# Optimization experiments

Measured on AMD Instinct MI355X. Metric: run time of the kernel, lower is better.

The kernel has to match this reference:

```python
import jax, jax.numpy as jnp
import numpy as np

N = 8192        # number of cells/nodes
D_IN = 30       # input feature dim
P_DIM = 3       # position dim
HID = 32        # attention hidden dim
D_OUT = 30      # backbone output dim
FF = 128        # MLP hidden width
SIGMA = 0.3     # spatial decay sigma


def setup_inputs() -> dict:
    key = jax.random.key(0)
    ks = jax.random.split(key, 12)
    w = lambda k, shape: (jax.random.normal(k, shape, jnp.float32) * 0.1)
    return {
        "t": jax.random.uniform(ks[0], (1,), jnp.float32),
        "Z": jax.random.normal(ks[1], (N, D_IN + P_DIM + 1), jnp.float32),
        # SpatialAttentionLayer params (Q/K/V projections + output proj)
        "Wq": w(ks[2], (D_IN, HID)), "bq": jnp.zeros((HID,), jnp.float32),
        "Wk": w(ks[3], (D_IN, HID)), "bk": jnp.zeros((HID,), jnp.float32),
        "Wv": w(ks[4], (D_IN, HID)), "bv": jnp.zeros((HID,), jnp.float32),
        "Wo": w(ks[5], (HID, D_OUT)), "bo": jnp.zeros((D_OUT,), jnp.float32),
        # LayerNorm
        "ln_g": jnp.ones((D_OUT,), jnp.float32), "ln_b": jnp.zeros((D_OUT,), jnp.float32),
        # backbone MLP: Linear(30,128) -> SiLU -> Linear(128,30)
        "W1": w(ks[6], (D_OUT, FF)), "b1": jnp.zeros((FF,), jnp.float32),
        "W2": w(ks[7], (FF, D_OUT)), "b2": jnp.zeros((D_OUT,), jnp.float32),
        # expr_head: Linear(30,30)
        "We": w(ks[8], (D_OUT, D_OUT)), "be": jnp.zeros((D_OUT,), jnp.float32),
    }


def reference(t, Z, Wq, bq, Wk, bk, Wv, bv, Wo, bo, ln_g, ln_b, W1, b1, W2, b2, We, be):
    # Z: (N, D_IN + P_DIM + 1); last column is kinetic energy (unused in fwd)
    X = Z[:, :-1]                       # (N, 33)
    P = X[:, -P_DIM:]                   # (N, 3) positions
    F = X[:, :D_IN]                     # (N, 30) features

    # --- SpatialAttentionLayer: sigma distance-decay attention, no softmax ---
    Q = F @ Wq + bq
    K = F @ Wk + bk
    V = F @ Wv + bv
    scores = (Q @ K.T) / jnp.sqrt(jnp.float32(HID))          # (N, N)
    pn = jnp.sum(P * P, axis=1)
    d2 = jnp.maximum(pn[:, None] + pn[None, :] - 2.0 * (P @ P.T), 0.0)
    decay = jnp.exp(-d2 / (2.0 * SIGMA * SIGMA))              # spatial decay kernel
    A = jax.nn.sigmoid(scores) * decay                        # no-softmax attention
    A = A / (jnp.sum(A, axis=1, keepdims=True) + 1e-8)        # row-normalized message passing
    H = (A @ V) @ Wo + bo                                     # (N, D_OUT)

    # --- LayerNorm(output_dim) ---
    mu = jnp.mean(H, axis=-1, keepdims=True)
    var = jnp.mean((H - mu) ** 2, axis=-1, keepdims=True)
    Hn = (H - mu) * jax.lax.rsqrt(var + 1e-5) * ln_g + ln_b

    # --- Linear(30,128) -> SiLU -> Linear(128,30) ---
    H2 = jax.nn.silu(Hn @ W1 + b1) @ W2 + b2

    # --- expr_head ---
    feature_velo = H2 @ We + be                               # (N, 30)

    # static_pos=True -> zero position velocities (velocity_head bypassed)
    pos_velo = jnp.zeros_like(P)                              # (N, 3)

    # kinetic energy term
    ke = 0.5 * jnp.mean(feature_velo ** 2, axis=1) + 0.5 * jnp.mean(pos_velo ** 2, axis=1)
    return jnp.concatenate([feature_velo, pos_velo, ke[:, None]], axis=1)  # (N, 34)
```

## Files before the change

### kernel.cpp

```cpp
#include <hip/hip_runtime.h>
#include <hip/hip_bf16.h>

#define N      8192
#define D_IN   30
#define HID    32
#define D_OUT  30
#define FFD    128
#define ZC     34
#define JGC    16

typedef __attribute__((ext_vector_type(8))) short short8;
typedef __attribute__((ext_vector_type(16))) float f32x16;

static __device__ __forceinline__ ushort f2bf(float x) {
    uint32_t u = __float_as_uint(x);
    uint32_t r = (u + 0x7fffu + ((u >> 16) & 1u)) >> 16;
    return (ushort)r;
}
static __device__ __forceinline__ float bf2f(ushort u) {
    return __uint_as_float(((uint32_t)u) << 16);
}

__global__ __launch_bounds__(256) void dv_qkv_kernel(
    const float* __restrict__ Z,
    const float* __restrict__ Wq, const float* __restrict__ bq,
    const float* __restrict__ Wk, const float* __restrict__ bk,
    const float* __restrict__ Wv, const float* __restrict__ bv,
    const float* __restrict__ Wo,
    const float* __restrict__ W2, const float* __restrict__ We,
    const float* __restrict__ b2, const float* __restrict__ be,
    ushort* __restrict__ Qb, ushort* __restrict__ Kb,
    ushort* __restrict__ VWot, ushort* __restrict__ KA,
    ushort* __restrict__ QB, float* __restrict__ W2e, float* __restrict__ b2e)
{
    __shared__ ushort sv[8][33];
    const int t = blockIdx.x * 256 + threadIdx.x;
    const int i = t >> 5;
    const int h = t & 31;
    const float* z = Z + (size_t)i * ZC;

    float q = bq[h], k = bk[h], v = bv[h];
#pragma unroll
    for (int d = 0; d < D_IN; ++d) {
        float zf = z[d];
        q = fmaf(zf, Wq[d * HID + h], q);
        k = fmaf(zf, Wk[d * HID + h], k);
        v = fmaf(zf, Wv[d * HID + h], v);
    }
    const float QS = 0.17677669529663687f * 1.4426950408889634f;
    Qb[(size_t)i * HID + h] = f2bf(q * QS);
    Kb[(size_t)i * HID + h] = f2bf(k);
    sv[threadIdx.x >> 5][h] = f2bf(v);

    if (h == 0) {
        float p0 = z[D_IN], p1 = z[D_IN + 1], p2 = z[D_IN + 2];
        const float C2 = 1.4426950408889634f / 0.18f;
        const float SC = sqrtf(2.0f * C2);
        float px = p0 * SC, py = p1 * SC, pz = p2 * SC;
        float w  = -C2 * (p0 * p0 + p1 * p1 + p2 * p2);
        ushort phx = f2bf(px), phy = f2bf(py), phz = f2bf(pz);
        ushort plx = f2bf(px - bf2f(phx));
        ushort ply = f2bf(py - bf2f(phy));
        ushort plz = f2bf(pz - bf2f(phz));
        ushort wh  = f2bf(w);
        ushort wl  = f2bf(w - bf2f(wh));
        ushort nhx = phx ^ 0x8000, nhy = phy ^ 0x8000, nhz = phz ^ 0x8000;
        ushort nlx = plx ^ 0x8000, nly = ply ^ 0x8000, nlz = plz ^ 0x8000;
        ushort nwh = wh ^ 0x8000,  nwl = wl ^ 0x8000;
        const ushort one = 0x3F80, none = 0xBF80;
        ushort ka0[8] = {nwh, nwl, none, none, nhx, nhy, nhz, nhx};
        ushort ka1[8] = {nhy, nhz, nlx, nly, nlz, nlx, nly, nlz};
        ushort qb0[8] = {one, one, wh, wl, phx, phy, phz, plx};
        ushort qb1[8] = {ply, plz, phx, phy, phz, plx, ply, plz};
        *(uint4*)&KA[(size_t)i * 8]       = *(uint4*)ka0;
        *(uint4*)&KA[((size_t)N + i) * 8] = *(uint4*)ka1;
        *(uint4*)&QB[(size_t)i * 8]       = *(uint4*)qb0;
        *(uint4*)&QB[((size_t)N + i) * 8] = *(uint4*)qb1;
    }

    if (blockIdx.x < 15) {
        int idx = blockIdx.x * 256 + threadIdx.x;
        int f = idx / 30, o = idx - f * 30;
        float acc = 0.f;
#pragma unroll
        for (int d = 0; d < D_OUT; ++d)
            acc = fmaf(W2[f * D_OUT + d], We[d * D_OUT + o], acc);
        W2e[idx] = acc;
        if (idx < D_OUT) {
            float a2 = be[idx];
#pragma unroll
            for (int d = 0; d < D_OUT; ++d)
                a2 = fmaf(b2[d], We[d * D_OUT + idx], a2);
            b2e[idx] = a2;
        }
    }

    __syncthreads();
    const int io = threadIdx.x >> 5, c = threadIdx.x & 31;
    const int ii = blockIdx.x * 8 + io;
    float val;
    if (c < 30) {
        float acc = 0.f;
#pragma unroll
        for (int hh = 0; hh < HID; ++hh)
            acc = fmaf(bf2f(sv[io][hh]), Wo[hh * D_OUT + c], acc);
        val = acc;
    } else {
        val = (c == 31) ? 1.0f : 0.f;
    }
    VWot[(size_t)c * N + ii] = f2bf(val);
}

__global__ __launch_bounds__(256, 2) void dv_attn_kernel(
    const ushort* __restrict__ Qb, const ushort* __restrict__ Kb,
    const ushort* __restrict__ VWot, const ushort* __restrict__ KA,
    const ushort* __restrict__ QB, float* __restrict__ partial, int nch)
{
    __shared__ ushort lK[128 * 32];
    __shared__ ushort lV[32 * 128];
    __shared__ ushort lKA[2][128 * 8];

    const int tid  = threadIdx.x;
    const int lane = tid & 63;
    const int wv   = tid >> 6;
    const int h2   = lane >> 5;
    const int l31  = lane & 31;
    const int rb   = blockIdx.x & 63;
    const int jg   = blockIdx.x >> 6;
    const int i0w  = rb * 128 + wv * 32;

    const ushort* qp = Qb + (size_t)(i0w + l31) * HID + h2 * 8;
    const short8 qf0 = *(const short8*)qp;
    const short8 qf1 = *(const short8*)(qp + 16);
    const short8 qaug = *(const short8*)&QB[((size_t)h2 * N + i0w + l31) * 8];

    f32x16 zacc, oacc;
#pragma unroll
    for (int r = 0; r < 16; ++r) { zacc[r] = 0.f; oacc[r] = 0.f; }

    const int cA0 = (h2 + (l31 >> 1)) & 3;
    const int cA1 = (cA0 + 2) & 3;

    const int kjr0 = tid >> 2,          kcc0 = tid & 3;
    const int kjr1 = (tid + 256) >> 2,  kcc1 = (tid + 256) & 3;
    const int kc20 = (kcc0 + (kjr0 >> 1)) & 3;
    const int kc21 = (kcc1 + (kjr1 >> 1)) & 3;
    const int vhh[4] = { tid >> 5, (tid + 256) >> 5, (tid + 512) >> 5, (tid + 768) >> 5 };
    const int vcc[4] = { tid & 31, tid & 31, tid & 31, tid & 31 };
    const int ahalf = tid >> 7, ajj = tid & 127;

    uint4 kreg[2];
    uint2 vreg[4];
    uint4 kareg;

    {
        const int j0 = (jg * nch) << 7;
        kreg[0] = *(const uint4*)&Kb[(size_t)(j0 + kjr0) * HID + kcc0 * 8];
        kreg[1] = *(const uint4*)&Kb[(size_t)(j0 + kjr1) * HID + kcc1 * 8];
#pragma unroll
        for (int r2 = 0; r2 < 4; ++r2)
            vreg[r2] = *(const uint2*)&VWot[(size_t)vhh[r2] * N + j0 + vcc[r2] * 4];
        kareg = *(const uint4*)&KA[((size_t)ahalf * N + j0 + ajj) * 8];
    }

    for (int ch = 0; ch < nch; ++ch) {
        __syncthreads();
        *(uint4*)&lK[kjr0 * 32 + kc20 * 8] = kreg[0];
        *(uint4*)&lK[kjr1 * 32 + kc21 * 8] = kreg[1];
#pragma unroll
        for (int r2 = 0; r2 < 4; ++r2)
            *(uint2*)&lV[vhh[r2] * 128 + (vcc[r2] ^ vhh[r2]) * 4] = vreg[r2];
        *(uint4*)&lKA[ahalf][ajj * 8] = kareg;
        __syncthreads();

        if (ch + 1 < nch) {
            const int j1 = (jg * nch + ch + 1) << 7;
            kreg[0] = *(const uint4*)&Kb[(size_t)(j1 + kjr0) * HID + kcc0 * 8];
            kreg[1] = *(const uint4*)&Kb[(size_t)(j1 + kjr1) * HID + kcc1 * 8];
#pragma unroll
            for (int r2 = 0; r2 < 4; ++r2)
                vreg[r2] = *(const uint2*)&VWot[(size_t)vhh[r2] * N + j1 + vcc[r2] * 4];
            kareg = *(const uint4*)&KA[((size_t)ahalf * N + j1 + ajj) * 8];
        }

#pragma unroll
        for (int t32 = 0; t32 < 4; ++t32) {
            const ushort* krow = &lK[(t32 * 32 + l31) * 32];
            short8 kf0 = *(const short8*)&krow[cA0 * 8];
            short8 kf1 = *(const short8*)&krow[cA1 * 8];
            f32x16 s = __builtin_amdgcn_mfma_f32_32x32x16_bf16(kf0, qf0, zacc, 0, 0, 0);
            s = __builtin_amdgcn_mfma_f32_32x32x16_bf16(kf1, qf1, s, 0, 0, 0);

            short8 kaug = *(const short8*)&lKA[h2][(t32 * 32 + l31) * 8];
            f32x16 gA = __builtin_amdgcn_mfma_f32_32x32x16_bf16(kaug, qaug, zacc, 0, 0, 0);

            uint32_t pk[8];
#pragma unroll
            for (int p = 0; p < 8; ++p) {
                float d0 = fmaxf(gA[2 * p], 0.f);
                float d1 = fmaxf(gA[2 * p + 1], 0.f);
                float eg0 = __builtin_amdgcn_exp2f(-d0);
                float es0 = __builtin_amdgcn_exp2f(-s[2 * p]);
                float a0  = eg0 * __builtin_amdgcn_rcpf(1.0f + es0);
                float eg1 = __builtin_amdgcn_exp2f(-d1);
                float es1 = __builtin_amdgcn_exp2f(-s[2 * p + 1]);
                float a1  = eg1 * __builtin_amdgcn_rcpf(1.0f + es1);
                asm("v_cvt_pk_bf16_f32 %0, %1, %2" : "=v"(pk[p]) : "v"(a0), "v"(a1));
            }
            union BV { uint32_t u[4]; short8 v; };
            BV fa, fb;
            fa.u[0] = pk[0]; fa.u[1] = pk[1]; fa.u[2] = pk[2]; fa.u[3] = pk[3];
            fb.u[0] = pk[4]; fb.u[1] = pk[5]; fb.u[2] = pk[6]; fb.u[3] = pk[7];

            const ushort* vrow = &lV[l31 * 128];
            const int cb = t32 * 8 + h2;
            BV b0, b1;
            *(uint2*)&b0.u[0] = *(const uint2*)&vrow[((cb    ) ^ l31) * 4];
            *(uint2*)&b0.u[2] = *(const uint2*)&vrow[((cb + 2) ^ l31) * 4];
            *(uint2*)&b1.u[0] = *(const uint2*)&vrow[((cb + 4) ^ l31) * 4];
            *(uint2*)&b1.u[2] = *(const uint2*)&vrow[((cb + 6) ^ l31) * 4];

            oacc = __builtin_amdgcn_mfma_f32_32x32x16_bf16(fa.v, b0.v, oacc, 0, 0, 0);
            oacc = __builtin_amdgcn_mfma_f32_32x32x16_bf16(fb.v, b1.v, oacc, 0, 0, 0);
        }
    }

#pragma unroll
    for (int r = 0; r < 16; ++r) {
        int ir = (r & 3) + 8 * (r >> 2) + 4 * h2 + i0w;
        partial[(size_t)ir * (JGC * 32) + jg * 32 + l31] = oacc[r];
    }
}

__global__ __launch_bounds__(256) void dv_epilogue_kernel(
    const float* __restrict__ partial,
    const float* __restrict__ bo,
    const float* __restrict__ ln_g, const float* __restrict__ ln_b,
    const float* __restrict__ W1, const float* __restrict__ b1,
    const float* __restrict__ W2e, const float* __restrict__ b2e,
    float* __restrict__ out)
{
    __shared__ float sr [32 * 16];
    __shared__ float sHl[30 * 16];
    __shared__ float sHn[30 * 16];
    __shared__ float shf[128 * 16];
    __shared__ float sker[16 * 16];

    const int tid  = threadIdx.x;
    const int row0 = blockIdx.x * 16;

#pragma unroll
    for (int rep = 0; rep < 2; ++rep) {
        int idx = tid + rep * 256;
        int r = idx >> 5, c = idx & 31;
        const float* pp = partial + (size_t)(row0 + r) * (JGC * 32) + c;
        float s = 0.f;
#pragma unroll
        for (int jg = 0; jg < JGC; ++jg)
            s += pp[jg * 32];
        sr[c * 16 + r] = s;
    }
    __syncthreads();

    const int rl  = tid & 15, grp = tid >> 4;
    const int o0  = grp * 2;
    const bool g15 = grp < 15;

    if (g15) {
        float inv = __builtin_amdgcn_rcpf(sr[31 * 16 + rl] + 1e-8f);
        float2 bb = *(const float2*)&bo[o0];
        sHl[(o0    ) * 16 + rl] = fmaf(sr[(o0    ) * 16 + rl], inv, bb.x);
        sHl[(o0 + 1) * 16 + rl] = fmaf(sr[(o0 + 1) * 16 + rl], inv, bb.y);
    }
    __syncthreads();

    if (tid < 16) {
        const int r = tid;
        float mu = 0.f;
#pragma unroll
        for (int o = 0; o < D_OUT; ++o) mu += sHl[o * 16 + r];
        mu *= (1.0f / D_OUT);
        float var = 0.f;
#pragma unroll
        for (int o = 0; o < D_OUT; ++o) {
            float d = sHl[o * 16 + r] - mu; var = fmaf(d, d, var);
        }
        float rs = rsqrtf(var * (1.0f / D_OUT) + 1e-5f);
#pragma unroll
        for (int o = 0; o < D_OUT; ++o)
            sHn[o * 16 + r] = fmaf((sHl[o * 16 + r] - mu) * rs, ln_g[o], ln_b[o]);
    }
    __syncthreads();

    {
        const int f0 = grp * 8;
        float acc[8];
        float4 b4a = *(const float4*)&b1[f0];
        float4 b4b = *(const float4*)&b1[f0 + 4];
        acc[0] = b4a.x; acc[1] = b4a.y; acc[2] = b4a.z; acc[3] = b4a.w;
        acc[4] = b4b.x; acc[5] = b4b.y; acc[6] = b4b.z; acc[7] = b4b.w;
#pragma unroll
        for (int o = 0; o < D_OUT; ++o) {
            float4 wa = *(const float4*)&W1[o * FFD + f0];
            float4 wb = *(const float4*)&W1[o * FFD + f0 + 4];
            float hn = sHn[o * 16 + rl];
            acc[0] = fmaf(hn, wa.x, acc[0]); acc[1] = fmaf(hn, wa.y, acc[1]);
            acc[2] = fmaf(hn, wa.z, acc[2]); acc[3] = fmaf(hn, wa.w, acc[3]);
            acc[4] = fmaf(hn, wb.x, acc[4]); acc[5] = fmaf(hn, wb.y, acc[5]);
            acc[6] = fmaf(hn, wb.z, acc[6]); acc[7] = fmaf(hn, wb.w, acc[7]);
        }
        const float L2E = 1.4426950408889634f;
#pragma unroll
        for (int ff = 0; ff < 8; ++ff) {
            float a = acc[ff];
            shf[(f0 + ff) * 16 + rl] =
                a * __builtin_amdgcn_rcpf(1.0f + __builtin_amdgcn_exp2f(-a * L2E));
        }
    }
    __syncthreads();

    if (g15) {
        float2 bb = *(const float2*)&b2e[o0];
        float a0 = bb.x, a1 = bb.y;
#pragma unroll 8
        for (int f = 0; f < FFD; ++f) {
            float2 w = *(const float2*)&W2e[f * D_OUT + o0];
            float hf = shf[f * 16 + rl];
            a0 = fmaf(hf, w.x, a0); a1 = fmaf(hf, w.y, a1);
        }
        float* op = out + (size_t)(row0 + rl) * ZC;
        op[o0] = a0; op[o0 + 1] = a1;
        sker[grp * 16 + rl] = fmaf(a0, a0, a1 * a1);
    }
    __syncthreads();

    if (tid < 16) {
        float ke = 0.f;
#pragma unroll
        for (int g = 0; g < 15; ++g) ke += sker[g * 16 + tid];
        float* op = out + (size_t)(row0 + tid) * ZC;
        op[30] = 0.f; op[31] = 0.f; op[32] = 0.f;
        op[33] = ke * (0.5f / D_OUT);
    }
}

extern "C" void kernel_launch(void* const* d_in, const int* in_sizes, int n_in,
                              void* d_out, int out_size, void* d_ws, size_t ws_size,
                              hipStream_t stream)
{
    const float* Z  = (const float*)d_in[1];
    const float* Wq = (const float*)d_in[2];
    const float* bq = (const float*)d_in[3];
    const float* Wk = (const float*)d_in[4];
    const float* bk = (const float*)d_in[5];
    const float* Wv = (const float*)d_in[6];
    const float* bv = (const float*)d_in[7];
    const float* Wo = (const float*)d_in[8];
    const float* bo = (const float*)d_in[9];
    const float* lg = (const float*)d_in[10];
    const float* lb = (const float*)d_in[11];
    const float* W1 = (const float*)d_in[12];
    const float* b1 = (const float*)d_in[13];
    const float* W2 = (const float*)d_in[14];
    const float* b2 = (const float*)d_in[15];
    const float* We = (const float*)d_in[16];
    const float* be = (const float*)d_in[17];
    float* out = (float*)d_out;

    ushort* Qb   = (ushort*)d_ws;
    ushort* Kb   = Qb + (size_t)N * HID;
    ushort* VWot = Kb + (size_t)N * HID;
    ushort* KA   = VWot + (size_t)N * HID;
    ushort* QB   = KA + (size_t)N * 16;
    float*  W2e  = (float*)(QB + (size_t)N * 16);
    float*  b2e  = W2e + FFD * D_OUT;
    float*  partial = b2e + 32;

    int nch = N / (JGC * 128);

    hipLaunchKernelGGL(dv_qkv_kernel, dim3((N * HID) / 256), dim3(256), 0, stream,
                       Z, Wq, bq, Wk, bk, Wv, bv, Wo, W2, We, b2, be,
                       Qb, Kb, VWot, KA, QB, W2e, b2e);
    hipLaunchKernelGGL(dv_attn_kernel, dim3(64 * JGC), dim3(256), 0, stream,
                       Qb, Kb, VWot, KA, QB, partial, nch);
    hipLaunchKernelGGL(dv_epilogue_kernel, dim3(N / 16), dim3(256), 0, stream,
                       partial, bo, lg, lb, W1, b1, W2e, b2e, out);
}
```

Measured before the change: 61.77 us.

## Rewrite epilogue as one wavefront per row and drop the distance clamp

Measured after the change: 58.44 us. -5.4%, faster.

```diff
diff --git a/kernel.cpp b/kernel.cpp
--- a/kernel.cpp
+++ b/kernel.cpp
@@ -19,6 +19,9 @@
 }
 static __device__ __forceinline__ float bf2f(ushort u) {
     return __uint_as_float(((uint32_t)u) << 16);
+}
+static __device__ __forceinline__ float rdlane(float v, int l) {
+    return __uint_as_float(__builtin_amdgcn_readlane(__float_as_uint(v), l));
 }
 
 __global__ __launch_bounds__(256) void dv_qkv_kernel(
@@ -146,7 +149,7 @@
     const int kc20 = (kcc0 + (kjr0 >> 1)) & 3;
     const int kc21 = (kcc1 + (kjr1 >> 1)) & 3;
     const int vhh[4] = { tid >> 5, (tid + 256) >> 5, (tid + 512) >> 5, (tid + 768) >> 5 };
-    const int vcc[4] = { tid & 31, tid & 31, tid & 31, tid & 31 };
+    const int vcx = tid & 31;
     const int ahalf = tid >> 7, ajj = tid & 127;
 
     uint4 kreg[2];
@@ -159,7 +162,7 @@
         kreg[1] = *(const uint4*)&Kb[(size_t)(j0 + kjr1) * HID + kcc1 * 8];
 #pragma unroll
         for (int r2 = 0; r2 < 4; ++r2)
-            vreg[r2] = *(const uint2*)&VWot[(size_t)vhh[r2] * N + j0 + vcc[r2] * 4];
+            vreg[r2] = *(const uint2*)&VWot[(size_t)vhh[r2] * N + j0 + vcx * 4];
         kareg = *(const uint4*)&KA[((size_t)ahalf * N + j0 + ajj) * 8];
     }
 
@@ -169,7 +172,7 @@
         *(uint4*)&lK[kjr1 * 32 + kc21 * 8] = kreg[1];
 #pragma unroll
         for (int r2 = 0; r2 < 4; ++r2)
-            *(uint2*)&lV[vhh[r2] * 128 + (vcc[r2] ^ vhh[r2]) * 4] = vreg[r2];
+            *(uint2*)&lV[vhh[r2] * 128 + (vcx ^ vhh[r2]) * 4] = vreg[r2];
         *(uint4*)&lKA[ahalf][ajj * 8] = kareg;
         __syncthreads();
 
@@ -179,7 +182,7 @@
             kreg[1] = *(const uint4*)&Kb[(size_t)(j1 + kjr1) * HID + kcc1 * 8];
 #pragma unroll
             for (int r2 = 0; r2 < 4; ++r2)
-                vreg[r2] = *(const uint2*)&VWot[(size_t)vhh[r2] * N + j1 + vcc[r2] * 4];
+                vreg[r2] = *(const uint2*)&VWot[(size_t)vhh[r2] * N + j1 + vcx * 4];
             kareg = *(const uint4*)&KA[((size_t)ahalf * N + j1 + ajj) * 8];
         }
 
@@ -197,12 +200,10 @@
             uint32_t pk[8];
 #pragma unroll
             for (int p = 0; p < 8; ++p) {
-                float d0 = fmaxf(gA[2 * p], 0.f);
-                float d1 = fmaxf(gA[2 * p + 1], 0.f);
-                float eg0 = __builtin_amdgcn_exp2f(-d0);
+                float eg0 = __builtin_amdgcn_exp2f(-gA[2 * p]);
                 float es0 = __builtin_amdgcn_exp2f(-s[2 * p]);
                 float a0  = eg0 * __builtin_amdgcn_rcpf(1.0f + es0);
-                float eg1 = __builtin_amdgcn_exp2f(-d1);
+                float eg1 = __builtin_amdgcn_exp2f(-gA[2 * p + 1]);
                 float es1 = __builtin_amdgcn_exp2f(-s[2 * p + 1]);
                 float a1  = eg1 * __builtin_amdgcn_rcpf(1.0f + es1);
                 asm("v_cvt_pk_bf16_f32 %0, %1, %2" : "=v"(pk[p]) : "v"(a0), "v"(a1));
@@ -240,107 +241,78 @@
     const float* __restrict__ W2e, const float* __restrict__ b2e,
     float* __restrict__ out)
 {
-    __shared__ float sr [32 * 16];
-    __shared__ float sHl[30 * 16];
-    __shared__ float sHn[30 * 16];
-    __shared__ float shf[128 * 16];
-    __shared__ float sker[16 * 16];
+    __shared__ float shf[4][FFD];
 
     const int tid  = threadIdx.x;
-    const int row0 = blockIdx.x * 16;
-
-#pragma unroll
-    for (int rep = 0; rep < 2; ++rep) {
-        int idx = tid + rep * 256;
-        int r = idx >> 5, c = idx & 31;
-        const float* pp = partial + (size_t)(row0 + r) * (JGC * 32) + c;
-        float s = 0.f;
-#pragma unroll
-        for (int jg = 0; jg < JGC; ++jg)
-            s += pp[jg * 32];
-        sr[c * 16 + r] = s;
-    }
-    __syncthreads();
-
-    const int rl  = tid & 15, grp = tid >> 4;
-    const int o0  = grp * 2;
-    const bool g15 = grp < 15;
-
-    if (g15) {
-        float inv = __builtin_amdgcn_rcpf(sr[31 * 16 + rl] + 1e-8f);
-        float2 bb = *(const float2*)&bo[o0];
-        sHl[(o0    ) * 16 + rl] = fmaf(sr[(o0    ) * 16 + rl], inv, bb.x);
-        sHl[(o0 + 1) * 16 + rl] = fmaf(sr[(o0 + 1) * 16 + rl], inv, bb.y);
-    }
-    __syncthreads();
-
-    if (tid < 16) {
-        const int r = tid;
-        float mu = 0.f;
-#pragma unroll
-        for (int o = 0; o < D_OUT; ++o) mu += sHl[o * 16 + r];
-        mu *= (1.0f / D_OUT);
-        float var = 0.f;
-#pragma unroll
-        for (int o = 0; o < D_OUT; ++o) {
-            float d = sHl[o * 16 + r] - mu; var = fmaf(d, d, var);
+    const int wv   = tid >> 6;
+    const int lane = tid & 63;
+    const int row  = blockIdx.x * 4 + wv;
+    const int c    = lane & 31;
+    const bool a30 = c < 30;
+    const int  c30 = a30 ? c : 0;
+
+    float s8 = 0.f;
+    {
+        const float* pp = partial + (size_t)row * (JGC * 32) + lane;
+#pragma unroll
+        for (int q = 0; q < 8; ++q) s8 += pp[q * 64];
+    }
+    float sv = s8 + __shfl_xor(s8, 32, 64);
+
+    float rsum = __shfl(sv, 31, 32);
+    float inv  = __builtin_amdgcn_rcpf(rsum + 1e-8f);
+    float Hl   = a30 ? fmaf(sv, inv, bo[c30]) : 0.f;
+
+    float x = Hl;
+#pragma unroll
+    for (int m = 1; m < 32; m <<= 1) x += __shfl_xor(x, m, 32);
+    float mu = x * (1.0f / D_OUT);
+    float d  = a30 ? (Hl - mu) : 0.f;
+    float v2 = d * d;
+#pragma unroll
+    for (int m = 1; m < 32; m <<= 1) v2 += __shfl_xor(v2, m, 32);
+    float rs = rsqrtf(v2 * (1.0f / D_OUT) + 1e-5f);
+    float Hn = fmaf(d * rs, ln_g[c30], ln_b[c30]);
+
+    float acc0 = b1[lane], acc1 = b1[lane + 64];
+#pragma unroll
+    for (int o = 0; o < D_OUT; ++o) {
+        float ho = rdlane(Hn, o);
+        acc0 = fmaf(ho, W1[o * FFD + lane], acc0);
+        acc1 = fmaf(ho, W1[o * FFD + lane + 64], acc1);
+    }
+    const float L2E = 1.4426950408889634f;
+    shf[wv][lane] =
+        acc0 * __builtin_amdgcn_rcpf(1.0f + __builtin_amdgcn_exp2f(-acc0 * L2E));
+    shf[wv][lane + 64] =
+        acc1 * __builtin_amdgcn_rcpf(1.0f + __builtin_amdgcn_exp2f(-acc1 * L2E));
+
+    const int half = lane >> 5;
+    float acc = 0.f;
+    {
+        const float* hbase = &shf[wv][half * 64];
+#pragma unroll
+        for (int k = 0; k < 16; ++k) {
+            float4 hv = *(const float4*)&hbase[k * 4];
+            const int f0 = half * 64 + k * 4;
+            acc = fmaf(hv.x, W2e[(f0    ) * D_OUT + c30], acc);
+            acc = fmaf(hv.y, W2e[(f0 + 1) * D_OUT + c30], acc);
+            acc = fmaf(hv.z, W2e[(f0 + 2) * D_OUT + c30], acc);
+            acc = fmaf(hv.w, W2e[(f0 + 3) * D_OUT + c30], acc);
         }
-        float rs = rsqrtf(var * (1.0f / D_OUT) + 1e-5f);
-#pragma unroll
-        for (int o = 0; o < D_OUT; ++o)
-            sHn[o * 16 + r] = fmaf((sHl[o * 16 + r] - mu) * rs, ln_g[o], ln_b[o]);
-    }
-    __syncthreads();
-
-    {
-        const int f0 = grp * 8;
-        float acc[8];
-        float4 b4a = *(const float4*)&b1[f0];
-        float4 b4b = *(const float4*)&b1[f0 + 4];
-        acc[0] = b4a.x; acc[1] = b4a.y; acc[2] = b4a.z; acc[3] = b4a.w;
-        acc[4] = b4b.x; acc[5] = b4b.y; acc[6] = b4b.z; acc[7] = b4b.w;
-#pragma unroll
-        for (int o = 0; o < D_OUT; ++o) {
-            float4 wa = *(const float4*)&W1[o * FFD + f0];
-            float4 wb = *(const float4*)&W1[o * FFD + f0 + 4];
-            float hn = sHn[o * 16 + rl];
-            acc[0] = fmaf(hn, wa.x, acc[0]); acc[1] = fmaf(hn, wa.y, acc[1]);
-            acc[2] = fmaf(hn, wa.z, acc[2]); acc[3] = fmaf(hn, wa.w, acc[3]);
-            acc[4] = fmaf(hn, wb.x, acc[4]); acc[5] = fmaf(hn, wb.y, acc[5]);
-            acc[6] = fmaf(hn, wb.z, acc[6]); acc[7] = fmaf(hn, wb.w, acc[7]);
-        }
-        const float L2E = 1.4426950408889634f;
-#pragma unroll
-        for (int ff = 0; ff < 8; ++ff) {
-            float a = acc[ff];
-            shf[(f0 + ff) * 16 + rl] =
-                a * __builtin_amdgcn_rcpf(1.0f + __builtin_amdgcn_exp2f(-a * L2E));
-        }
-    }
-    __syncthreads();
-
-    if (g15) {
-        float2 bb = *(const float2*)&b2e[o0];
-        float a0 = bb.x, a1 = bb.y;
-#pragma unroll 8
-        for (int f = 0; f < FFD; ++f) {
-            float2 w = *(const float2*)&W2e[f * D_OUT + o0];
-            float hf = shf[f * 16 + rl];
-            a0 = fmaf(hf, w.x, a0); a1 = fmaf(hf, w.y, a1);
-        }
-        float* op = out + (size_t)(row0 + rl) * ZC;
-        op[o0] = a0; op[o0 + 1] = a1;
-        sker[grp * 16 + rl] = fmaf(a0, a0, a1 * a1);
-    }
-    __syncthreads();
-
-    if (tid < 16) {
-        float ke = 0.f;
-#pragma unroll
-        for (int g = 0; g < 15; ++g) ke += sker[g * 16 + tid];
-        float* op = out + (size_t)(row0 + tid) * ZC;
+    }
+    float val = acc + __shfl_xor(acc, 32, 64) + b2e[c30];
+
+    if (lane < 32 && a30)
+        out[(size_t)row * ZC + c] = val;
+
+    float kep = a30 ? val * val : 0.f;
+#pragma unroll
+    for (int m = 1; m < 32; m <<= 1) kep += __shfl_xor(kep, m, 32);
+    if (lane == 0) {
+        float* op = out + (size_t)row * ZC;
         op[30] = 0.f; op[31] = 0.f; op[32] = 0.f;
-        op[33] = ke * (0.5f / D_OUT);
+        op[33] = kep * (0.5f / D_OUT);
     }
 }
 
@@ -383,6 +355,6 @@
                        Qb, Kb, VWot, KA, QB, W2e, b2e);
     hipLaunchKernelGGL(dv_attn_kernel, dim3(64 * JGC), dim3(256), 0, stream,
                        Qb, Kb, VWot, KA, QB, partial, nch);
-    hipLaunchKernelGGL(dv_epilogue_kernel, dim3(N / 16), dim3(256), 0, stream,
+    hipLaunchKernelGGL(dv_epilogue_kernel, dim3(N / 4), dim3(256), 0, stream,
                        partial, bo, lg, lb, W1, b1, W2e, b2e, out);
 }
```
